# Performance work log

Measured on AMD Instinct MI355X. Metric: run time of the kernel, lower is better.

## Reference

```python
import jax, jax.numpy as jnp
import numpy as np

NODE_SIZE = 100000
RELATION_SIZE = 8
D = 64  # node_embed_size
B = 65536


def setup_inputs() -> dict:
    key = jax.random.key(0)
    k1, k2, k3, k4, k5 = jax.random.split(key, 5)
    node_idx = jax.random.randint(k1, (B,), 0, NODE_SIZE)
    relation_idx = jax.random.randint(k2, (B,), 0, RELATION_SIZE)
    node_neighbor_idx = jax.random.randint(k3, (B,), 0, NODE_SIZE)
    node_table = jax.random.normal(k4, (NODE_SIZE, D), dtype=jnp.float32)
    # xavier_uniform on [relation_size, D*D]
    limit = np.sqrt(6.0 / (RELATION_SIZE + D * D))
    relation_table = jax.random.uniform(k5, (RELATION_SIZE, D * D), dtype=jnp.float32,
                                        minval=-limit, maxval=limit)
    return {"node_idx": node_idx, "relation_idx": relation_idx,
            "node_neighbor_idx": node_neighbor_idx,
            "node_table": node_table, "relation_table": relation_table}


def reference(node_idx, relation_idx, node_neighbor_idx, node_table, relation_table):
    node_embed = node_table[node_idx]                     # [B, D]
    rel = relation_table[relation_idx].reshape(-1, D, D)  # [B, D, D]
    temp = jnp.einsum('bd,bde->be', node_embed, rel)      # (B,1,D)@(B,D,D) squeezed
    neighbor = node_table[node_neighbor_idx]              # [B, D]
    score = jnp.sum(temp * neighbor, axis=-1, keepdims=True)  # [B, 1]
    return jax.nn.sigmoid(score)
```

## Files before the change

### kernel.cpp

```cpp
#include <hip/hip_runtime.h>
#include <cstdint>

#define DIM 64
#define NREL 8
#define IPB 128
#define CAP 48
#define NTHREADS 512

typedef __attribute__((ext_vector_type(8))) short short8;
typedef __attribute__((ext_vector_type(4))) float f32x4;

__device__ __forceinline__ uint32_t cvtpk_bf16(float lo, float hi) {
    uint32_t r;
    asm("v_cvt_pk_bf16_f32 %0, %1, %2" : "=v"(r) : "v"(lo), "v"(hi));
    return r;
}

__global__ __launch_bounds__(NTHREADS, 4) void fused_kernel(
    const int* __restrict__ node_idx,
    const int* __restrict__ rel_idx,
    const int* __restrict__ nb_idx,
    const float* __restrict__ node_table,
    const float* __restrict__ rel_table,
    float* __restrict__ out, int B)
{
    __shared__ int4 dslot[NREL][CAP];
    __shared__ int  wcnt[8][NREL];
    __shared__ int  tcnt[NREL];

    int tid  = threadIdx.x;
    int lane = tid & 63;
    int wv   = tid >> 6;

    int i = blockIdx.x * IPB + tid;
    bool active = (tid < IPB) && (i < B);
    int r = active ? rel_idx[i] : -1;

    unsigned long long mymask = 0;
#pragma unroll
    for (int rr = 0; rr < NREL; ++rr) {
        unsigned long long mk = __ballot(r == rr);
        if (lane == 0) wcnt[wv][rr] = (int)__popcll(mk);
        if (rr == r) mymask = mk;
    }
    __syncthreads();

    if (tid < NREL) {
        int tot = 0;
#pragma unroll
        for (int w = 0; w < 8; ++w) {
            int c = wcnt[w][tid];
            wcnt[w][tid] = tot;
            tot += c;
        }
        tcnt[tid] = tot;
    }
    __syncthreads();

    if (active) {
        int rank = (int)__popcll(mymask & ((1ull << lane) - 1ull));
        int pos = wcnt[wv][r] + rank;
        if (pos < CAP) {
            int4 q;
            q.x = node_idx[i];
            q.y = nb_idx[i];
            q.z = i;
            q.w = 0;
            dslot[r][pos] = q;
        }
    }
    __syncthreads();

    int n = tcnt[wv];
    if (n > CAP) n = CAP;
    if (n == 0) return;

    int lg = lane >> 4;
    int li = lane & 15;

    const float* Rb = rel_table + ((size_t)wv << 12);
    short8 Bf[2][4];
#pragma unroll
    for (int kt = 0; kt < 2; ++kt) {
#pragma unroll
        for (int nt = 0; nt < 4; ++nt) {
            const float* p = Rb + (size_t)(kt * 32 + lg * 8) * DIM + nt * 16 + li;
            float g0 = p[0 * DIM], g1 = p[1 * DIM], g2 = p[2 * DIM], g3 = p[3 * DIM];
            float g4 = p[4 * DIM], g5 = p[5 * DIM], g6 = p[6 * DIM], g7 = p[7 * DIM];
            union { uint32_t u[4]; short8 s; } f;
            f.u[0] = cvtpk_bf16(g0, g1);
            f.u[1] = cvtpk_bf16(g2, g3);
            f.u[2] = cvtpk_bf16(g4, g5);
            f.u[3] = cvtpk_bf16(g6, g7);
            Bf[kt][nt] = f.s;
        }
    }

#pragma unroll 1
    for (int base = 0; base < n; base += 16) {
        int rem = n - base;
        if (rem > 16) rem = 16;

        int4 qa = dslot[wv][base + ((li < rem) ? li : (rem - 1))];
        const float* mrow = node_table + (size_t)qa.x * DIM;
        short8 Af[2];
#pragma unroll
        for (int kt = 0; kt < 2; ++kt) {
            const float* mp = mrow + kt * 32 + lg * 8;
            f32x4 lo = *(const f32x4*)(mp);
            f32x4 hi = *(const f32x4*)(mp + 4);
            union { uint32_t u[4]; short8 s; } f;
            f.u[0] = cvtpk_bf16(lo.x, lo.y);
            f.u[1] = cvtpk_bf16(lo.z, lo.w);
            f.u[2] = cvtpk_bf16(hi.x, hi.y);
            f.u[3] = cvtpk_bf16(hi.z, hi.w);
            Af[kt] = f.s;
        }

        f32x4 acc[4];
#pragma unroll
        for (int nt = 0; nt < 4; ++nt) {
            f32x4 z = {0.f, 0.f, 0.f, 0.f};
            acc[nt] = __builtin_amdgcn_mfma_f32_16x16x32_bf16(Af[0], Bf[0][nt], z, 0, 0, 0);
            acc[nt] = __builtin_amdgcn_mfma_f32_16x16x32_bf16(Af[1], Bf[1][nt], acc[nt], 0, 0, 0);
        }

        int4 qj[4];
#pragma unroll
        for (int jr = 0; jr < 4; ++jr) {
            int idx = lg * 4 + jr;
            qj[jr] = dslot[wv][base + ((idx < rem) ? idx : (rem - 1))];
        }

        float s0 = 0.f, s1 = 0.f, s2 = 0.f, s3 = 0.f;
#pragma unroll
        for (int nt = 0; nt < 4; ++nt) {
            int eoff = nt * 16 + li;
            s0 = fmaf(acc[nt].x, node_table[(size_t)qj[0].y * DIM + eoff], s0);
            s1 = fmaf(acc[nt].y, node_table[(size_t)qj[1].y * DIM + eoff], s1);
            s2 = fmaf(acc[nt].z, node_table[(size_t)qj[2].y * DIM + eoff], s2);
            s3 = fmaf(acc[nt].w, node_table[(size_t)qj[3].y * DIM + eoff], s3);
        }
#pragma unroll
        for (int off = 1; off < 16; off <<= 1) {
            s0 += __shfl_xor(s0, off, 64);
            s1 += __shfl_xor(s1, off, 64);
            s2 += __shfl_xor(s2, off, 64);
            s3 += __shfl_xor(s3, off, 64);
        }

        if (li == 0) {
            if (lg * 4 + 0 < rem) out[qj[0].z] = 1.0f / (1.0f + __expf(-s0));
            if (lg * 4 + 1 < rem) out[qj[1].z] = 1.0f / (1.0f + __expf(-s1));
            if (lg * 4 + 2 < rem) out[qj[2].z] = 1.0f / (1.0f + __expf(-s2));
            if (lg * 4 + 3 < rem) out[qj[3].z] = 1.0f / (1.0f + __expf(-s3));
        }
    }
}

extern "C" void kernel_launch(void* const* d_in, const int* in_sizes, int n_in,
                              void* d_out, int out_size, void* d_ws, size_t ws_size,
                              hipStream_t stream) {
    const int*   node_idx   = (const int*)d_in[0];
    const int*   rel_idx    = (const int*)d_in[1];
    const int*   nb_idx     = (const int*)d_in[2];
    const float* node_table = (const float*)d_in[3];
    const float* rel_table  = (const float*)d_in[4];
    float* out = (float*)d_out;
    int B = in_sizes[0];

    int blocks = (B + IPB - 1) / IPB;
    fused_kernel<<<blocks, NTHREADS, 0, stream>>>(node_idx, rel_idx, nb_idx,
                                                  node_table, rel_table, out, B);
}
```

Baseline: 14.55 us.

## Shrink blocks to one wave of items, overlap relation loads with bucketing

Halves items per block to 64 so a single wave can bucket items by relation with ballots. This removes the cross-wave prefix scan and two of the three block barriers, and CAP now equals IPB so no item can overflow a bucket. The relation-matrix loads are issued before the bucketing so their latency overlaps it. Neighbor-row and node-row loads are hoisted ahead of the MFMAs to overlap memory latency. The cost is twice as many blocks, each reloading the full 8x4K relation table, and more live registers per thread.

```diff
diff --git a/kernel.cpp b/kernel.cpp
--- a/kernel.cpp
+++ b/kernel.cpp
@@ -3,8 +3,8 @@
 
 #define DIM 64
 #define NREL 8
-#define IPB 128
-#define CAP 48
+#define IPB 64
+#define CAP 64
 #define NTHREADS 512
 
 typedef __attribute__((ext_vector_type(8))) short short8;
@@ -25,76 +25,65 @@
     float* __restrict__ out, int B)
 {
     __shared__ int4 dslot[NREL][CAP];
-    __shared__ int  wcnt[8][NREL];
     __shared__ int  tcnt[NREL];
 
     int tid  = threadIdx.x;
     int lane = tid & 63;
     int wv   = tid >> 6;
 
-    int i = blockIdx.x * IPB + tid;
-    bool active = (tid < IPB) && (i < B);
-    int r = active ? rel_idx[i] : -1;
-
-    unsigned long long mymask = 0;
-#pragma unroll
-    for (int rr = 0; rr < NREL; ++rr) {
-        unsigned long long mk = __ballot(r == rr);
-        if (lane == 0) wcnt[wv][rr] = (int)__popcll(mk);
-        if (rr == r) mymask = mk;
-    }
-    __syncthreads();
-
-    if (tid < NREL) {
-        int tot = 0;
-#pragma unroll
-        for (int w = 0; w < 8; ++w) {
-            int c = wcnt[w][tid];
-            wcnt[w][tid] = tot;
-            tot += c;
-        }
-        tcnt[tid] = tot;
-    }
-    __syncthreads();
-
-    if (active) {
-        int rank = (int)__popcll(mymask & ((1ull << lane) - 1ull));
-        int pos = wcnt[wv][r] + rank;
-        if (pos < CAP) {
-            int4 q;
-            q.x = node_idx[i];
-            q.y = nb_idx[i];
-            q.z = i;
-            q.w = 0;
-            dslot[r][pos] = q;
-        }
-    }
-    __syncthreads();
-
-    int n = tcnt[wv];
-    if (n > CAP) n = CAP;
-    if (n == 0) return;
-
     int lg = lane >> 4;
     int li = lane & 15;
 
     const float* Rb = rel_table + ((size_t)wv << 12);
-    short8 Bf[2][4];
+    float g[2][4][8];
 #pragma unroll
-    for (int kt = 0; kt < 2; ++kt) {
+    for (int kt = 0; kt < 2; ++kt)
 #pragma unroll
         for (int nt = 0; nt < 4; ++nt) {
             const float* p = Rb + (size_t)(kt * 32 + lg * 8) * DIM + nt * 16 + li;
-            float g0 = p[0 * DIM], g1 = p[1 * DIM], g2 = p[2 * DIM], g3 = p[3 * DIM];
-            float g4 = p[4 * DIM], g5 = p[5 * DIM], g6 = p[6 * DIM], g7 = p[7 * DIM];
+#pragma unroll
+            for (int j = 0; j < 8; ++j)
+                g[kt][nt][j] = p[j * DIM];
+        }
+
+    if (wv == 0) {
+        int i = blockIdx.x * IPB + lane;
+        bool act = i < B;
+        int r  = act ? rel_idx[i]  : -1;
+        int ni = act ? node_idx[i] : 0;
+        int mi = act ? nb_idx[i]   : 0;
+
+        unsigned long long mymask = 0;
+#pragma unroll
+        for (int rr = 0; rr < NREL; ++rr) {
+            unsigned long long mk = __ballot(r == rr);
+            if (lane == rr) tcnt[rr] = (int)__popcll(mk);
+            if (rr == r) mymask = mk;
+        }
+        if (act) {
+            int rank = (int)__popcll(mymask & ((1ull << lane) - 1ull));
+            int4 q; q.x = ni; q.y = mi; q.z = i; q.w = 0;
+            dslot[r][rank] = q;
+        }
+    }
+
+    short8 Bf[2][4];
+#pragma unroll
+    for (int kt = 0; kt < 2; ++kt)
+#pragma unroll
+        for (int nt = 0; nt < 4; ++nt) {
             union { uint32_t u[4]; short8 s; } f;
-            f.u[0] = cvtpk_bf16(g0, g1);
-            f.u[1] = cvtpk_bf16(g2, g3);
-            f.u[2] = cvtpk_bf16(g4, g5);
-            f.u[3] = cvtpk_bf16(g6, g7);
+            f.u[0] = cvtpk_bf16(g[kt][nt][0], g[kt][nt][1]);
+            f.u[1] = cvtpk_bf16(g[kt][nt][2], g[kt][nt][3]);
+            f.u[2] = cvtpk_bf16(g[kt][nt][4], g[kt][nt][5]);
+            f.u[3] = cvtpk_bf16(g[kt][nt][6], g[kt][nt][7]);
             Bf[kt][nt] = f.s;
         }
-    }
+
+    __syncthreads();
+
+    int n = tcnt[wv];
+    if (n == 0) return;
 
 #pragma unroll 1
     for (int base = 0; base < n; base += 16) {
@@ -102,19 +91,39 @@
         if (rem > 16) rem = 16;
 
         int4 qa = dslot[wv][base + ((li < rem) ? li : (rem - 1))];
+        int4 qj[4];
+#pragma unroll
+        for (int jr = 0; jr < 4; ++jr) {
+            int idx = lg * 4 + jr;
+            qj[jr] = dslot[wv][base + ((idx < rem) ? idx : (rem - 1))];
+        }
+
         const float* mrow = node_table + (size_t)qa.x * DIM;
+        f32x4 lo0 = *(const f32x4*)(mrow + lg * 8);
+        f32x4 hi0 = *(const f32x4*)(mrow + lg * 8 + 4);
+        f32x4 lo1 = *(const f32x4*)(mrow + 32 + lg * 8);
+        f32x4 hi1 = *(const f32x4*)(mrow + 32 + lg * 8 + 4);
+
+        float nval[4][4];
+#pragma unroll
+        for (int jr = 0; jr < 4; ++jr)
+#pragma unroll
+            for (int nt = 0; nt < 4; ++nt)
+                nval[jr][nt] = node_table[(size_t)qj[jr].y * DIM + nt * 16 + li];
+
         short8 Af[2];
-#pragma unroll
-        for (int kt = 0; kt < 2; ++kt) {
-            const float* mp = mrow + kt * 32 + lg * 8;
-            f32x4 lo = *(const f32x4*)(mp);
-            f32x4 hi = *(const f32x4*)(mp + 4);
+        {
             union { uint32_t u[4]; short8 s; } f;
-            f.u[0] = cvtpk_bf16(lo.x, lo.y);
-            f.u[1] = cvtpk_bf16(lo.z, lo.w);
-            f.u[2] = cvtpk_bf16(hi.x, hi.y);
-            f.u[3] = cvtpk_bf16(hi.z, hi.w);
-            Af[kt] = f.s;
+            f.u[0] = cvtpk_bf16(lo0.x, lo0.y);
+            f.u[1] = cvtpk_bf16(lo0.z, lo0.w);
+            f.u[2] = cvtpk_bf16(hi0.x, hi0.y);
+            f.u[3] = cvtpk_bf16(hi0.z, hi0.w);
+            Af[0] = f.s;
+            f.u[0] = cvtpk_bf16(lo1.x, lo1.y);
+            f.u[1] = cvtpk_bf16(lo1.z, lo1.w);
+            f.u[2] = cvtpk_bf16(hi1.x, hi1.y);
+            f.u[3] = cvtpk_bf16(hi1.z, hi1.w);
+            Af[1] = f.s;
         }
 
         f32x4 acc[4];
@@ -125,21 +134,13 @@
             acc[nt] = __builtin_amdgcn_mfma_f32_16x16x32_bf16(Af[1], Bf[1][nt], acc[nt], 0, 0, 0);
         }
 
-        int4 qj[4];
-#pragma unroll
-        for (int jr = 0; jr < 4; ++jr) {
-            int idx = lg * 4 + jr;
-            qj[jr] = dslot[wv][base + ((idx < rem) ? idx : (rem - 1))];
-        }
-
         float s0 = 0.f, s1 = 0.f, s2 = 0.f, s3 = 0.f;
 #pragma unroll
         for (int nt = 0; nt < 4; ++nt) {
-            int eoff = nt * 16 + li;
-            s0 = fmaf(acc[nt].x, node_table[(size_t)qj[0].y * DIM + eoff], s0);
-            s1 = fmaf(acc[nt].y, node_table[(size_t)qj[1].y * DIM + eoff], s1);
-            s2 = fmaf(acc[nt].z, node_table[(size_t)qj[2].y * DIM + eoff], s2);
-            s3 = fmaf(acc[nt].w, node_table[(size_t)qj[3].y * DIM + eoff], s3);
+            s0 = fmaf(acc[nt].x, nval[0][nt], s0);
+            s1 = fmaf(acc[nt].y, nval[1][nt], s1);
+            s2 = fmaf(acc[nt].z, nval[2][nt], s2);
+            s3 = fmaf(acc[nt].w, nval[3][nt], s3);
         }
 #pragma unroll
         for (int off = 1; off < 16; off <<= 1) {
```

Result: slower. 16.38 us (+12.6%).
